# Performance work log

Hardware: AMD Instinct MI355X
Metric: run time of the kernel (lower is better)

Reference implementation:

```python
import jax, jax.numpy as jnp
import numpy as np

N_V = 100000   # vertices
N_E = 20000    # hyperedges
N_PAIRS = 1600000  # incidence pairs
F = 128
H = 128
EPS = 1e-5


def setup_inputs() -> dict:
    key = jax.random.key(0)
    k1, k2, k3, k4 = jax.random.split(key, 4)
    X = jax.random.normal(k1, (N_V, F), dtype=jnp.float32)
    vertex_ids = jax.random.randint(k2, (N_PAIRS,), 0, N_V, dtype=jnp.int32)
    edge_ids = jax.random.randint(k3, (N_PAIRS,), 0, N_E, dtype=jnp.int32)
    W = jax.random.normal(k4, (F, H), dtype=jnp.float32) * (1.0 / np.sqrt(F))
    b = jnp.zeros((H,), dtype=jnp.float32)
    gamma = jnp.ones((H,), dtype=jnp.float32)
    beta = jnp.zeros((H,), dtype=jnp.float32)
    return {"X": X, "vertex_ids": vertex_ids, "edge_ids": edge_ids,
            "W": W, "b": b, "gamma": gamma, "beta": beta}


def _segment_mean(vals, ids, num_segments):
    s = jax.ops.segment_sum(vals, ids, num_segments=num_segments)
    cnt = jax.ops.segment_sum(jnp.ones((ids.shape[0], 1), vals.dtype), ids,
                              num_segments=num_segments)
    return s / jnp.maximum(cnt, 1.0)


def reference(X, vertex_ids, edge_ids, W, b, gamma, beta):
    # linear: theta
    h = X @ W + b                                    # [N_V, H]
    # batchnorm (batch statistics, as in training mode)
    mu = jnp.mean(h, axis=0)
    var = jnp.var(h, axis=0)
    h = (h - mu) * jax.lax.rsqrt(var + EPS) * gamma + beta
    # hypergraph v2v mean: vertex -> hyperedge mean, then hyperedge -> vertex mean
    Xe = _segment_mean(h[vertex_ids], edge_ids, N_E)   # [N_E, H]
    Xv = _segment_mean(Xe[edge_ids], vertex_ids, N_V)  # [N_V, H]
    # activation (ReLU); dropout is identity in eval
    return jax.nn.relu(Xv)
```

## Files before the change

### kernel.cpp

```cpp
#include <hip/hip_runtime.h>
#include <hip/hip_bf16.h>

#define N_V 100000
#define N_E 20000
#define N_P 1600000
#define FDIM 128
#define HDIM 128
#define BN_EPS 1e-5f

#define SORT_C 4096
#define SORT_BLOCKS ((N_P + SORT_C - 1) / SORT_C)
#define NB_E 313
#define EB_SHIFT 6
#define EB_REGION 9216
#define EB_SORT 5888
#define NB_V 391
#define VB_SHIFT 8
#define VB_REGION 8192
#define VB_SORT 4608
#define SENTINEL 0xFFFFFFFFu

#define EIDX_CAP 192
#define VIDX_CAP 64

typedef __attribute__((ext_vector_type(8))) short short8;
typedef __attribute__((ext_vector_type(4))) float floatx4;

__device__ __forceinline__ float bf_lo(unsigned u) {
    return __uint_as_float(u << 16);
}
__device__ __forceinline__ float bf_hi(unsigned u) {
    return __uint_as_float(u & 0xffff0000u);
}
__device__ __forceinline__ unsigned short f2bf(float f) {
    unsigned u = __float_as_uint(f);
    return (unsigned short)((u + 0x7fffu + ((u >> 16) & 1u)) >> 16);
}

__device__ __forceinline__ void acc4(float* s, const uint2& u) {
    s[0] += bf_lo(u.x); s[1] += bf_hi(u.x);
    s[2] += bf_lo(u.y); s[3] += bf_hi(u.y);
}

__device__ __forceinline__ void acc8(float* s, const uint4& u) {
    s[0] += bf_lo(u.x); s[1] += bf_hi(u.x);
    s[2] += bf_lo(u.y); s[3] += bf_hi(u.y);
    s[4] += bf_lo(u.z); s[5] += bf_hi(u.z);
    s[6] += bf_lo(u.w); s[7] += bf_hi(u.w);
}

#define GEMM_BLOCKS 625
#define WT_STRIDE 136
__global__ __launch_bounds__(256) void k_gemm_mfma(
    const float* __restrict__ X, const float* __restrict__ W,
    const float* __restrict__ bias, unsigned* __restrict__ h_u) {
    __shared__ unsigned short WTs[FDIM * WT_STRIDE];
    const int t = threadIdx.x;
    for (int idx = t; idx < FDIM * HDIM; idx += 256) {
        const int k = idx >> 7, m = idx & 127;
        WTs[m * WT_STRIDE + k] = f2bf(W[idx]);
    }
    __syncthreads();

    const int wave = t >> 6, lane = t & 63;
    const int quad = lane >> 4, sub = lane & 15;
    const int nstrips = N_V / 16;

    for (int s = blockIdx.x * 4 + wave; s < nstrips; s += GEMM_BLOCKS * 4) {
        const int row0 = s * 16;
        short8 xf[4];
        const float* xp = X + (size_t)(row0 + sub) * FDIM + quad * 8;
        #pragma unroll
        for (int kt = 0; kt < 4; ++kt) {
            const float4 a = *(const float4*)(xp + kt * 32);
            const float4 b2 = *(const float4*)(xp + kt * 32 + 4);
            short8 f;
            f[0] = (short)f2bf(a.x);  f[1] = (short)f2bf(a.y);
            f[2] = (short)f2bf(a.z);  f[3] = (short)f2bf(a.w);
            f[4] = (short)f2bf(b2.x); f[5] = (short)f2bf(b2.y);
            f[6] = (short)f2bf(b2.z); f[7] = (short)f2bf(b2.w);
            xf[kt] = f;
        }
        #pragma unroll
        for (int tile = 0; tile < 8; ++tile) {
            floatx4 acc = {0.f, 0.f, 0.f, 0.f};
            const unsigned short* wp =
                WTs + (tile * 16 + sub) * WT_STRIDE + quad * 8;
            #pragma unroll
            for (int kt = 0; kt < 4; ++kt) {
                const short8 af = *(const short8*)(wp + kt * 32);
                acc = __builtin_amdgcn_mfma_f32_16x16x32_bf16(af, xf[kt], acc,
                                                              0, 0, 0);
            }
            const int ch = tile * 16 + quad * 4;
            const float4 bb = *(const float4*)(bias + ch);
            const float c0 = acc[0] + bb.x, c1 = acc[1] + bb.y;
            const float c2 = acc[2] + bb.z, c3 = acc[3] + bb.w;
            const unsigned lo = (unsigned)f2bf(c0) | ((unsigned)f2bf(c1) << 16);
            const unsigned hi = (unsigned)f2bf(c2) | ((unsigned)f2bf(c3) << 16);
            uint2* dst = (uint2*)(h_u + (size_t)(row0 + sub) * 64 + (ch >> 1));
            *dst = make_uint2(lo, hi);
        }
    }
}

#define BN_BLOCKS 400
#define BN_RPB 250
__global__ __launch_bounds__(256) void k_bn_stats(
    const unsigned* __restrict__ h_u, float* __restrict__ sums ) {
    const int t = threadIdx.x;
    const int c8 = t & 15;
    const int rw = t >> 4;
    const int r0 = blockIdx.x * BN_RPB;
    const int r1 = min(r0 + BN_RPB, N_V);
    float s[8] = {0.f,0.f,0.f,0.f,0.f,0.f,0.f,0.f};
    float ss[8] = {0.f,0.f,0.f,0.f,0.f,0.f,0.f,0.f};
    for (int r = r0 + rw; r < r1; r += 16) {
        const uint4 u = *(const uint4*)(h_u + (size_t)r * 64 + c8 * 4);
        const float x0 = bf_lo(u.x), x1 = bf_hi(u.x);
        const float x2 = bf_lo(u.y), x3 = bf_hi(u.y);
        const float x4 = bf_lo(u.z), x5 = bf_hi(u.z);
        const float x6 = bf_lo(u.w), x7 = bf_hi(u.w);
        s[0]+=x0; ss[0]+=x0*x0;  s[1]+=x1; ss[1]+=x1*x1;
        s[2]+=x2; ss[2]+=x2*x2;  s[3]+=x3; ss[3]+=x3*x3;
        s[4]+=x4; ss[4]+=x4*x4;  s[5]+=x5; ss[5]+=x5*x5;
        s[6]+=x6; ss[6]+=x6*x6;  s[7]+=x7; ss[7]+=x7*x7;
    }
    #pragma unroll
    for (int k = 0; k < 8; ++k) {
        s[k]  += __shfl_xor(s[k], 16);  s[k]  += __shfl_xor(s[k], 32);
        ss[k] += __shfl_xor(ss[k], 16); ss[k] += __shfl_xor(ss[k], 32);
    }
    __shared__ float ls[128], lss[128];
    for (int k = t; k < 128; k += 256) { ls[k] = 0.f; lss[k] = 0.f; }
    __syncthreads();
    if ((t & 63) < 16) {
        #pragma unroll
        for (int k = 0; k < 8; ++k) {
            atomicAdd(&ls[c8 * 8 + k], s[k]);
            atomicAdd(&lss[c8 * 8 + k], ss[k]);
        }
    }
    __syncthreads();
    if (t < 128) {
        atomicAdd(&sums[t],       ls[t]);
        atomicAdd(&sums[128 + t], lss[t]);
    }
}

__global__ void k_bn_final(const float* __restrict__ sums,
                           const float* __restrict__ gamma,
                           const float* __restrict__ beta,
                           float* __restrict__ scale, float* __restrict__ shift) {
    const int c = threadIdx.x;
    const float inv_n = 1.0f / (float)N_V;
    const float mu  = sums[c] * inv_n;
    const float var = sums[128 + c] * inv_n - mu * mu;
    const float inv = rsqrtf(var + BN_EPS);
    const float sc  = gamma[c] * inv;
    scale[c] = sc;
    shift[c] = beta[c] - mu * sc;
}

__global__ __launch_bounds__(256) void k_sort_dual(
    const int* __restrict__ vid, const int* __restrict__ eid,
    int* __restrict__ gcntE, int* __restrict__ gcntV,
    unsigned* __restrict__ partE, unsigned* __restrict__ partV) {
    __shared__ unsigned stageE[SORT_C];
    __shared__ unsigned stageV[SORT_C];
    __shared__ int histE[NB_E], curE[NB_E], offsE[NB_E], gbaseE[NB_E];
    __shared__ int histV[NB_V], curV[NB_V], offsV[NB_V], gbaseV[NB_V];
    __shared__ int partial[256];
    const int t = threadIdx.x;
    const int p0 = blockIdx.x * SORT_C;
    const int n = min(SORT_C, N_P - p0);
    const int n4 = n >> 2;
    const int4* e4p = (const int4*)(eid + p0);
    const int4* v4p = (const int4*)(vid + p0);

    for (int k = t; k < NB_E; k += 256) histE[k] = 0;
    for (int k = t; k < NB_V; k += 256) histV[k] = 0;
    __syncthreads();
    for (int i = t; i < n4; i += 256) {
        const int4 e4 = e4p[i];
        const int4 v4 = v4p[i];
        atomicAdd(&histE[((unsigned)e4.x) >> EB_SHIFT], 1);
        atomicAdd(&histE[((unsigned)e4.y) >> EB_SHIFT], 1);
        atomicAdd(&histE[((unsigned)e4.z) >> EB_SHIFT], 1);
        atomicAdd(&histE[((unsigned)e4.w) >> EB_SHIFT], 1);
        atomicAdd(&histV[((unsigned)v4.x) >> VB_SHIFT], 1);
        atomicAdd(&histV[((unsigned)v4.y) >> VB_SHIFT], 1);
        atomicAdd(&histV[((unsigned)v4.z) >> VB_SHIFT], 1);
        atomicAdd(&histV[((unsigned)v4.w) >> VB_SHIFT], 1);
    }
    __syncthreads();
    {
        constexpr int G = (NB_E + 255) / 256;
        int loc[G]; int s = 0;
        #pragma unroll
        for (int g = 0; g < G; ++g) {
            int idx = t * G + g; loc[g] = s;
            if (idx < NB_E) s += histE[idx];
        }
        partial[t] = s;
        __syncthreads();
        for (int d = 1; d < 256; d <<= 1) {
            int x = (t >= d) ? partial[t - d] : 0;
            __syncthreads(); partial[t] += x; __syncthreads();
        }
        const int base = t ? partial[t - 1] : 0;
        #pragma unroll
        for (int g = 0; g < G; ++g) {
            int idx = t * G + g;
            if (idx < NB_E) { offsE[idx] = base + loc[g]; curE[idx] = base + loc[g]; }
        }
        __syncthreads();
    }
    {
        constexpr int G = (NB_V + 255) / 256;
        int loc[G]; int s = 0;
        #pragma unroll
        for (int g = 0; g < G; ++g) {
            int idx = t * G + g; loc[g] = s;
            if (idx < NB_V) s += histV[idx];
        }
        partial[t] = s;
        __syncthreads();
        for (int d = 1; d < 256; d <<= 1) {
            int x = (t >= d) ? partial[t - d] : 0;
            __syncthreads(); partial[t] += x; __syncthreads();
        }
        const int base = t ? partial[t - 1] : 0;
        #pragma unroll
        for (int g = 0; g < G; ++g) {
            int idx = t * G + g;
            if (idx < NB_V) { offsV[idx] = base + loc[g]; curV[idx] = base + loc[g]; }
        }
        __syncthreads();
    }
    for (int i = t; i < n4; i += 256) {
        const int4 e4 = e4p[i];
        const int4 v4 = v4p[i];
        #pragma unroll
        for (int q = 0; q < 4; ++q) {
            const int ev = (q == 0) ? e4.x : (q == 1) ? e4.y : (q == 2) ? e4.z : e4.w;
            const int vv = (q == 0) ? v4.x : (q == 1) ? v4.y : (q == 2) ? v4.z : v4.w;
            const unsigned pkE = ((unsigned)(ev & 63) << 17) | (unsigned)vv;
            stageE[atomicAdd(&curE[(unsigned)ev >> EB_SHIFT], 1)] = pkE;
            const unsigned pkV = ((unsigned)(vv & 255) << 15) | (unsigned)ev;
            stageV[atomicAdd(&curV[(unsigned)vv >> VB_SHIFT], 1)] = pkV;
        }
    }
    __syncthreads();
    for (int k = t; k < NB_E; k += 256) {
        const int c = histE[k];
        gbaseE[k] = c ? atomicAdd(&gcntE[k], (c + 15) & ~15) : 0;
    }
    for (int k = t; k < NB_V; k += 256) {
        const int c = histV[k];
        gbaseV[k] = c ? atomicAdd(&gcntV[k], (c + 15) & ~15) : 0;
    }
    __syncthreads();
    for (int k = t >> 3; k < NB_E; k += 32) {
        const int c = histE[k];
        if (c == 0) continue;
        int cpad = (c + 15) & ~15;
        const int gb = gbaseE[k];
        if (gb >= EB_REGION) continue;
        cpad = min(cpad, EB_REGION - gb);
        unsigned* dst = partE + (size_t)k * EB_REGION + gb;
        const int lo = offsE[k];
        for (int j = (t & 7) * 4; j + 3 < cpad; j += 32) {
            uint4 w;
            w.x = (j + 0 < c) ? stageE[lo + j + 0] : SENTINEL;
            w.y = (j + 1 < c) ? stageE[lo + j + 1] : SENTINEL;
            w.z = (j + 2 < c) ? stageE[lo + j + 2] : SENTINEL;
            w.w = (j + 3 < c) ? stageE[lo + j + 3] : SENTINEL;
            *(uint4*)(dst + j) = w;
        }
    }
    for (int k = t >> 3; k < NB_V; k += 32) {
        const int c = histV[k];
        if (c == 0) continue;
        int cpad = (c + 15) & ~15;
        const int gb = gbaseV[k];
        if (gb >= VB_REGION) continue;
        cpad = min(cpad, VB_REGION - gb);
        unsigned* dst = partV + (size_t)k * VB_REGION + gb;
        const int lo = offsV[k];
        for (int j = (t & 7) * 4; j + 3 < cpad; j += 32) {
            uint4 w;
            w.x = (j + 0 < c) ? stageV[lo + j + 0] : SENTINEL;
            w.y = (j + 1 < c) ? stageV[lo + j + 1] : SENTINEL;
            w.z = (j + 2 < c) ? stageV[lo + j + 2] : SENTINEL;
            w.w = (j + 3 < c) ? stageV[lo + j + 3] : SENTINEL;
            *(uint4*)(dst + j) = w;
        }
    }
}

template <int NKEY, int PACK_SHIFT, int CAP, int REGION, int STRIDE>
__global__ __launch_bounds__(256) void k_csr(
    const unsigned* __restrict__ part, const int* __restrict__ gcnt,
    int nkeys_total, int* __restrict__ segoff, int* __restrict__ segcnt,
    unsigned* __restrict__ csr) {
    __shared__ __align__(16) unsigned B[CAP];
    __shared__ int hist[NKEY], offs[NKEY + 1], cur[NKEY];
    const int bkt = blockIdx.x;
    const int t = threadIdx.x;
    const unsigned mask = (1u << PACK_SHIFT) - 1u;
    const int tot = min(gcnt[bkt], REGION);
    const int tot4 = tot >> 2;
    const unsigned* src = part + (size_t)bkt * REGION;

    for (int k = t; k < NKEY; k += 256) { hist[k] = 0; cur[k] = 0; }
    __syncthreads();
    for (int i = t; i < tot4; i += 256) {
        const uint4 a = ((const uint4*)src)[i];
        if (a.x != SENTINEL) atomicAdd(&hist[a.x >> PACK_SHIFT], 1);
        if (a.y != SENTINEL) atomicAdd(&hist[a.y >> PACK_SHIFT], 1);
        if (a.z != SENTINEL) atomicAdd(&hist[a.z >> PACK_SHIFT], 1);
        if (a.w != SENTINEL) atomicAdd(&hist[a.w >> PACK_SHIFT], 1);
    }
    for (int i = tot4 * 4 + t; i < tot; i += 256) {
        const unsigned a = src[i];
        if (a != SENTINEL) atomicAdd(&hist[a >> PACK_SHIFT], 1);
    }
    __syncthreads();
    if (t == 0) {
        int acc = 0;
        for (int k = 0; k < NKEY; ++k) { offs[k] = acc; acc += hist[k]; }
        offs[NKEY] = acc;
    }
    __syncthreads();
    for (int i = t; i < tot4; i += 256) {
        const uint4 a = ((const uint4*)src)[i];
        #pragma unroll
        for (int q = 0; q < 4; ++q) {
            const unsigned av = (q == 0) ? a.x : (q == 1) ? a.y : (q == 2) ? a.z : a.w;
            if (av != SENTINEL) {
                const int k = av >> PACK_SHIFT;
                const int pos = offs[k] + atomicAdd(&cur[k], 1);
                if (pos < CAP) B[pos] = av & mask;
            }
        }
    }
    for (int i = tot4 * 4 + t; i < tot; i += 256) {
        const unsigned av = src[i];
        if (av != SENTINEL) {
            const int k = av >> PACK_SHIFT;
            const int pos = offs[k] + atomicAdd(&cur[k], 1);
            if (pos < CAP) B[pos] = av & mask;
        }
    }
    __syncthreads();
    const int total = min(offs[NKEY], CAP);
    unsigned* dst = csr + (size_t)bkt * STRIDE;
    for (int i = t * 4; i + 3 < total; i += 1024)
        *(uint4*)(dst + i) = *(const uint4*)(&B[i]);
    for (int i = (total & ~3) + t; i < total; i += 256) dst[i] = B[i];
    for (int k = t; k < NKEY; k += 256) {
        const int g = bkt * NKEY + k;
        if (g < nkeys_total) {
            const int o0 = min(offs[k], CAP);
            const int o1 = min(offs[k + 1], CAP);
            segoff[g] = bkt * STRIDE + o0;
            segcnt[g] = o1 - o0;
        }
    }
}

__global__ __launch_bounds__(256) void k_edge_gather(
    const unsigned* __restrict__ h_u, const unsigned* __restrict__ csrE,
    const int* __restrict__ eoff, const int* __restrict__ ecnt,
    const float* __restrict__ scale, const float* __restrict__ shift,
    unsigned* __restrict__ xe_u) {
    __shared__ int ib[4][EIDX_CAP];
    const int b = blockIdx.x;
    const int xcd = b & 7;
    const int half = xcd >> 2;
    const int grp = (b >> 3) * 4 + (xcd & 3);
    const int wave = threadIdx.x >> 6;
    const int e = grp * 4 + wave;
    const int l = threadIdx.x & 63;
    const int rg = l >> 4, c = l & 15;
    const int wbase = half * 32 + 2 * c;
    int o = 0, n = 0;
    if (e < N_E) { o = eoff[e]; n = ecnt[e]; }
    const int nc = min(n, EIDX_CAP);
    int* mi = ib[wave];
    for (int i = l; i < nc; i += 64) mi[i] = (int)csrE[o + i];
    __syncthreads();

    float s[4] = {0.f, 0.f, 0.f, 0.f};
    int j = 0;
    for (; j + 31 < nc; j += 32) {
        const int r0 = mi[j + rg],      r1 = mi[j + 4 + rg];
        const int r2 = mi[j + 8 + rg],  r3 = mi[j + 12 + rg];
        const int r4 = mi[j + 16 + rg], r5 = mi[j + 20 + rg];
        const int r6 = mi[j + 24 + rg], r7 = mi[j + 28 + rg];
        const uint2 u0 = *(const uint2*)(h_u + (size_t)r0 * 64 + wbase);
        const uint2 u1 = *(const uint2*)(h_u + (size_t)r1 * 64 + wbase);
        const uint2 u2 = *(const uint2*)(h_u + (size_t)r2 * 64 + wbase);
        const uint2 u3 = *(const uint2*)(h_u + (size_t)r3 * 64 + wbase);
        const uint2 u4 = *(const uint2*)(h_u + (size_t)r4 * 64 + wbase);
        const uint2 u5 = *(const uint2*)(h_u + (size_t)r5 * 64 + wbase);
        const uint2 u6 = *(const uint2*)(h_u + (size_t)r6 * 64 + wbase);
        const uint2 u7 = *(const uint2*)(h_u + (size_t)r7 * 64 + wbase);
        acc4(s, u0); acc4(s, u1); acc4(s, u2); acc4(s, u3);
        acc4(s, u4); acc4(s, u5); acc4(s, u6); acc4(s, u7);
    }
    for (; j + 15 < nc; j += 16) {
        const int r0 = mi[j + rg],     r1 = mi[j + 4 + rg];
        const int r2 = mi[j + 8 + rg], r3 = mi[j + 12 + rg];
        const uint2 u0 = *(const uint2*)(h_u + (size_t)r0 * 64 + wbase);
        const uint2 u1 = *(const uint2*)(h_u + (size_t)r1 * 64 + wbase);
        const uint2 u2 = *(const uint2*)(h_u + (size_t)r2 * 64 + wbase);
        const uint2 u3 = *(const uint2*)(h_u + (size_t)r3 * 64 + wbase);
        acc4(s, u0); acc4(s, u1); acc4(s, u2); acc4(s, u3);
    }
    for (; j < nc; j += 4) {
        if (j + rg < nc) {
            const int r = mi[j + rg];
            const uint2 u = *(const uint2*)(h_u + (size_t)r * 64 + wbase);
            acc4(s, u);
        }
    }
    for (int jj = nc; jj < n; jj += 4) {
        if (jj + rg < n) {
            const int r = (int)csrE[o + jj + rg];
            const uint2 u = *(const uint2*)(h_u + (size_t)r * 64 + wbase);
            acc4(s, u);
        }
    }
    #pragma unroll
    for (int k = 0; k < 4; ++k) {
        s[k] += __shfl_xor(s[k], 16);
        s[k] += __shfl_xor(s[k], 32);
    }
    if (e < N_E && rg == 0) {
        float m[4] = {0.f, 0.f, 0.f, 0.f};
        if (n > 0) {
            const float rc = 1.0f / (float)n;
            const float4 sc4 = ((const float4*)scale)[half * 16 + c];
            const float4 sh4 = ((const float4*)shift)[half * 16 + c];
            m[0] = sc4.x * s[0] * rc + sh4.x;
            m[1] = sc4.y * s[1] * rc + sh4.y;
            m[2] = sc4.z * s[2] * rc + sh4.z;
            m[3] = sc4.w * s[3] * rc + sh4.w;
        }
        uint2 pk;
        pk.x = (unsigned)f2bf(m[0]) | ((unsigned)f2bf(m[1]) << 16);
        pk.y = (unsigned)f2bf(m[2]) | ((unsigned)f2bf(m[3]) << 16);
        *(uint2*)(xe_u + (size_t)e * 64 + wbase) = pk;
    }
}

__global__ __launch_bounds__(256) void k_vert_gather(
    const unsigned* __restrict__ xe_u, const unsigned* __restrict__ csrV,
    const int* __restrict__ voff, const int* __restrict__ vcnt,
    float* __restrict__ out) {
    __shared__ int ib[4][VIDX_CAP];
    const int wave = threadIdx.x >> 6;
    const int v = blockIdx.x * 4 + wave;
    const int l = threadIdx.x & 63;
    const int g = l >> 4, c = l & 15;
    int o = 0, n = 0;
    if (v < N_V) { o = voff[v]; n = vcnt[v]; }
    const int nc = min(n, VIDX_CAP);
    int* mi = ib[wave];
    for (int i = l; i < nc; i += 64) mi[i] = (int)csrV[o + i];
    __syncthreads();

    float s[8] = {0.f, 0.f, 0.f, 0.f, 0.f, 0.f, 0.f, 0.f};
    int j = 0;
    for (; j + 15 < nc; j += 16) {
        const int r0 = mi[j + g],     r1 = mi[j + 4 + g];
        const int r2 = mi[j + 8 + g], r3 = mi[j + 12 + g];
        const uint4 u0 = *(const uint4*)(xe_u + (size_t)r0 * 64 + 4 * c);
        const uint4 u1 = *(const uint4*)(xe_u + (size_t)r1 * 64 + 4 * c);
        const uint4 u2 = *(const uint4*)(xe_u + (size_t)r2 * 64 + 4 * c);
        const uint4 u3 = *(const uint4*)(xe_u + (size_t)r3 * 64 + 4 * c);
        acc8(s, u0); acc8(s, u1); acc8(s, u2); acc8(s, u3);
    }
    for (; j < nc; j += 4) {
        if (j + g < nc) {
            const int r = mi[j + g];
            const uint4 u = *(const uint4*)(xe_u + (size_t)r * 64 + 4 * c);
            acc8(s, u);
        }
    }
    for (int jj = nc; jj < n; jj += 4) {
        if (jj + g < n) {
            const int r = (int)csrV[o + jj + g];
            const uint4 u = *(const uint4*)(xe_u + (size_t)r * 64 + 4 * c);
            acc8(s, u);
        }
    }
    #pragma unroll
    for (int k = 0; k < 8; ++k) {
        s[k] += __shfl_xor(s[k], 16);
        s[k] += __shfl_xor(s[k], 32);
    }
    if (v < N_V && g == 0) {
        const float rc = 1.0f / (float)max(n, 1);
        float4 r0, r1;
        r0.x = fmaxf(s[0] * rc, 0.f);
        r0.y = fmaxf(s[1] * rc, 0.f);
        r0.z = fmaxf(s[2] * rc, 0.f);
        r0.w = fmaxf(s[3] * rc, 0.f);
        r1.x = fmaxf(s[4] * rc, 0.f);
        r1.y = fmaxf(s[5] * rc, 0.f);
        r1.z = fmaxf(s[6] * rc, 0.f);
        r1.w = fmaxf(s[7] * rc, 0.f);
        ((float4*)out)[(size_t)v * 32 + 2 * c]     = r0;
        ((float4*)out)[(size_t)v * 32 + 2 * c + 1] = r1;
    }
}

extern "C" void kernel_launch(void* const* d_in, const int* in_sizes, int n_in,
                              void* d_out, int out_size, void* d_ws, size_t ws_size,
                              hipStream_t stream) {
    const float* X     = (const float*)d_in[0];
    const int*   vid   = (const int*)d_in[1];
    const int*   eid   = (const int*)d_in[2];
    const float* W     = (const float*)d_in[3];
    const float* b     = (const float*)d_in[4];
    const float* gamma = (const float*)d_in[5];
    const float* beta  = (const float*)d_in[6];
    float* out = (float*)d_out;

    char* ws = (char*)d_ws;
    unsigned* h_u   = (unsigned*)ws;  ws += (size_t)N_V * 64 * 4;
    unsigned* xe_u  = (unsigned*)ws;  ws += (size_t)N_E * 64 * 4;
    unsigned* partE = (unsigned*)ws;  ws += (size_t)NB_E * EB_REGION * 4;
    unsigned* partV = (unsigned*)ws;  ws += (size_t)NB_V * VB_REGION * 4;
    unsigned* csrE  = (unsigned*)ws;  ws += (size_t)NB_E * EB_SORT * 4;
    unsigned* csrV  = (unsigned*)ws;  ws += (size_t)NB_V * VB_SORT * 4;
    int* eoff = (int*)ws;             ws += (size_t)N_E * 4;
    int* ecnt = (int*)ws;             ws += (size_t)N_E * 4;
    int* voff = (int*)ws;             ws += (size_t)N_V * 4;
    int* vcnt = (int*)ws;             ws += (size_t)N_V * 4;
    char* zbase = ws;
    int*   gcntE = (int*)ws;          ws += (size_t)NB_E * 4;
    int*   gcntV = (int*)ws;          ws += (size_t)NB_V * 4;
    float* sums  = (float*)ws;        ws += 256 * 4;
    float* scale = (float*)ws;        ws += 128 * 4;
    float* shift = (float*)ws;        ws += 128 * 4;

    hipMemsetAsync(zbase, 0, (size_t)((char*)scale - zbase), stream);

    k_gemm_mfma<<<GEMM_BLOCKS, 256, 0, stream>>>(X, W, b, h_u);
    k_bn_stats<<<BN_BLOCKS, 256, 0, stream>>>(h_u, sums);
    k_bn_final<<<1, 128, 0, stream>>>(sums, gamma, beta, scale, shift);

    k_sort_dual<<<SORT_BLOCKS, 256, 0, stream>>>(vid, eid, gcntE, gcntV,
                                                 partE, partV);

    k_csr<64, 17, EB_SORT, EB_REGION, EB_SORT>
        <<<NB_E, 256, 0, stream>>>(partE, gcntE, N_E, eoff, ecnt, csrE);
    k_csr<256, 15, VB_SORT, VB_REGION, VB_SORT>
        <<<NB_V, 256, 0, stream>>>(partV, gcntV, N_V, voff, vcnt, csrV);

    k_edge_gather<<<(N_E / 4) * 2, 256, 0, stream>>>(h_u, csrE, eoff, ecnt,
                                                     scale, shift, xe_u);
    k_vert_gather<<<(N_V + 3) / 4, 256, 0, stream>>>(xe_u, csrV, voff, vcnt,
                                                     out);
}
```

Baseline: 285.3 us.

## Merge independent GEMM/sort and BN-stats/CSR stages into shared launches

Combines the GEMM kernel with the dual bucket-sort kernel into one launch whose blocks take one role or the other by block index, and likewise merges BN statistics with both CSR builds. Shared memory is overlaid with unions sized to the larger role. The aim is to cut launch count and let independent work fill the GPU at the same time rather than serialising small grids. The trade-off is that every block reserves the larger shared-memory footprint, which may reduce occupancy for the lighter role, and the mixed workloads may contend for memory bandwidth.

Result: faster. 259.2 us (-9.2%).

```diff
diff --git a/kernel.cpp b/kernel.cpp
--- a/kernel.cpp
+++ b/kernel.cpp
@@ -23,6 +23,11 @@
 #define EIDX_CAP 192
 #define VIDX_CAP 64
 
+#define GEMM_BLOCKS 625
+#define WT_STRIDE 136
+#define BN_BLOCKS 400
+#define BN_RPB 250
+
 typedef __attribute__((ext_vector_type(8))) short short8;
 typedef __attribute__((ext_vector_type(4))) float floatx4;
 
@@ -49,12 +54,36 @@
     s[6] += bf_lo(u.w); s[7] += bf_hi(u.w);
 }
 
-#define GEMM_BLOCKS 625
-#define WT_STRIDE 136
-__global__ __launch_bounds__(256) void k_gemm_mfma(
-    const float* __restrict__ X, const float* __restrict__ W,
-    const float* __restrict__ bias, unsigned* __restrict__ h_u) {
-    __shared__ unsigned short WTs[FDIM * WT_STRIDE];
+union SmemGemmSort {
+    struct {
+        unsigned short WTs[FDIM * WT_STRIDE];
+    } g;
+    struct {
+        unsigned stageE[SORT_C];
+        unsigned stageV[SORT_C];
+        int histE[NB_E], curE[NB_E], offsE[NB_E], gbaseE[NB_E];
+        int histV[NB_V], curV[NB_V], offsV[NB_V], gbaseV[NB_V];
+        int partial[256];
+    } s;
+};
+
+union SmemBnCsr {
+    struct {
+        unsigned B[EB_SORT];
+        int hist[256];
+        int offs[257];
+        int cur[256];
+    } c;
+    struct {
+        float ls[128], lss[128];
+    } b;
+};
+
+__device__ void gemm_body(int bid, unsigned short* WTs,
+                          const float* __restrict__ X,
+                          const float* __restrict__ W,
+                          const float* __restrict__ bias,
+                          unsigned* __restrict__ h_u) {
     const int t = threadIdx.x;
     for (int idx = t; idx < FDIM * HDIM; idx += 256) {
         const int k = idx >> 7, m = idx & 127;
@@ -66,7 +95,7 @@
     const int quad = lane >> 4, sub = lane & 15;
     const int nstrips = N_V / 16;
 
-    for (int s = blockIdx.x * 4 + wave; s < nstrips; s += GEMM_BLOCKS * 4) {
+    for (int s = bid * 4 + wave; s < nstrips; s += GEMM_BLOCKS * 4) {
         const int row0 = s * 16;
         short8 xf[4];
         const float* xp = X + (size_t)(row0 + sub) * FDIM + quad * 8;
@@ -104,75 +133,21 @@
     }
 }
 
-#define BN_BLOCKS 400
-#define BN_RPB 250
-__global__ __launch_bounds__(256) void k_bn_stats(
-    const unsigned* __restrict__ h_u, float* __restrict__ sums ) {
+__device__ void sort_body(int bid, SmemGemmSort* sm,
+                          const int* __restrict__ vid,
+                          const int* __restrict__ eid,
+                          int* __restrict__ gcntE, int* __restrict__ gcntV,
+                          unsigned* __restrict__ partE,
+                          unsigned* __restrict__ partV) {
+    unsigned* stageE = sm->s.stageE;
+    unsigned* stageV = sm->s.stageV;
+    int* histE = sm->s.histE; int* curE = sm->s.curE;
+    int* offsE = sm->s.offsE; int* gbaseE = sm->s.gbaseE;
+    int* histV = sm->s.histV; int* curV = sm->s.curV;
+    int* offsV = sm->s.offsV; int* gbaseV = sm->s.gbaseV;
+    int* partial = sm->s.partial;
     const int t = threadIdx.x;
-    const int c8 = t & 15;
-    const int rw = t >> 4;
-    const int r0 = blockIdx.x * BN_RPB;
-    const int r1 = min(r0 + BN_RPB, N_V);
-    float s[8] = {0.f,0.f,0.f,0.f,0.f,0.f,0.f,0.f};
-    float ss[8] = {0.f,0.f,0.f,0.f,0.f,0.f,0.f,0.f};
-    for (int r = r0 + rw; r < r1; r += 16) {
-        const uint4 u = *(const uint4*)(h_u + (size_t)r * 64 + c8 * 4);
-        const float x0 = bf_lo(u.x), x1 = bf_hi(u.x);
-        const float x2 = bf_lo(u.y), x3 = bf_hi(u.y);
-        const float x4 = bf_lo(u.z), x5 = bf_hi(u.z);
-        const float x6 = bf_lo(u.w), x7 = bf_hi(u.w);
-        s[0]+=x0; ss[0]+=x0*x0;  s[1]+=x1; ss[1]+=x1*x1;
-        s[2]+=x2; ss[2]+=x2*x2;  s[3]+=x3; ss[3]+=x3*x3;
-        s[4]+=x4; ss[4]+=x4*x4;  s[5]+=x5; ss[5]+=x5*x5;
-        s[6]+=x6; ss[6]+=x6*x6;  s[7]+=x7; ss[7]+=x7*x7;
-    }
-    #pragma unroll
-    for (int k = 0; k < 8; ++k) {
-        s[k]  += __shfl_xor(s[k], 16);  s[k]  += __shfl_xor(s[k], 32);
-        ss[k] += __shfl_xor(ss[k], 16); ss[k] += __shfl_xor(ss[k], 32);
-    }
-    __shared__ float ls[128], lss[128];
-    for (int k = t; k < 128; k += 256) { ls[k] = 0.f; lss[k] = 0.f; }
-    __syncthreads();
-    if ((t & 63) < 16) {
-        #pragma unroll
-        for (int k = 0; k < 8; ++k) {
-            atomicAdd(&ls[c8 * 8 + k], s[k]);
-            atomicAdd(&lss[c8 * 8 + k], ss[k]);
-        }
-    }
-    __syncthreads();
-    if (t < 128) {
-        atomicAdd(&sums[t],       ls[t]);
-        atomicAdd(&sums[128 + t], lss[t]);
-    }
-}
-
-__global__ void k_bn_final(const float* __restrict__ sums,
-                           const float* __restrict__ gamma,
-                           const float* __restrict__ beta,
-                           float* __restrict__ scale, float* __restrict__ shift) {
-    const int c = threadIdx.x;
-    const float inv_n = 1.0f / (float)N_V;
-    const float mu  = sums[c] * inv_n;
-    const float var = sums[128 + c] * inv_n - mu * mu;
-    const float inv = rsqrtf(var + BN_EPS);
-    const float sc  = gamma[c] * inv;
-    scale[c] = sc;
-    shift[c] = beta[c] - mu * sc;
-}
-
-__global__ __launch_bounds__(256) void k_sort_dual(
-    const int* __restrict__ vid, const int* __restrict__ eid,
-    int* __restrict__ gcntE, int* __restrict__ gcntV,
-    unsigned* __restrict__ partE, unsigned* __restrict__ partV) {
-    __shared__ unsigned stageE[SORT_C];
-    __shared__ unsigned stageV[SORT_C];
-    __shared__ int histE[NB_E], curE[NB_E], offsE[NB_E], gbaseE[NB_E];
-    __shared__ int histV[NB_V], curV[NB_V], offsV[NB_V], gbaseV[NB_V];
-    __shared__ int partial[256];
-    const int t = threadIdx.x;
-    const int p0 = blockIdx.x * SORT_C;
+    const int p0 = bid * SORT_C;
     const int n = min(SORT_C, N_P - p0);
     const int n4 = n >> 2;
     const int4* e4p = (const int4*)(eid + p0);
@@ -299,14 +274,68 @@
     }
 }
 
+__global__ __launch_bounds__(256) void k_gemm_sort(
+    const float* __restrict__ X, const float* __restrict__ W,
+    const float* __restrict__ bias, unsigned* __restrict__ h_u,
+    const int* __restrict__ vid, const int* __restrict__ eid,
+    int* __restrict__ gcntE, int* __restrict__ gcntV,
+    unsigned* __restrict__ partE, unsigned* __restrict__ partV) {
+    __shared__ __align__(16) SmemGemmSort sm;
+    const int b = blockIdx.x;
+    if (b < GEMM_BLOCKS)
+        gemm_body(b, sm.g.WTs, X, W, bias, h_u);
+    else
+        sort_body(b - GEMM_BLOCKS, &sm, vid, eid, gcntE, gcntV, partE, partV);
+}
+
+__device__ void bn_body(int bid, float* ls, float* lss,
+                        const unsigned* __restrict__ h_u,
+                        float* __restrict__ sums) {
+    const int t = threadIdx.x;
+    const int c8 = t & 15;
+    const int rw = t >> 4;
+    const int r0 = bid * BN_RPB;
+    const int r1 = min(r0 + BN_RPB, N_V);
+    float s[8] = {0.f,0.f,0.f,0.f,0.f,0.f,0.f,0.f};
+    float ss[8] = {0.f,0.f,0.f,0.f,0.f,0.f,0.f,0.f};
+    for (int r = r0 + rw; r < r1; r += 16) {
+        const uint4 u = *(const uint4*)(h_u + (size_t)r * 64 + c8 * 4);
+        const float x0 = bf_lo(u.x), x1 = bf_hi(u.x);
+        const float x2 = bf_lo(u.y), x3 = bf_hi(u.y);
+        const float x4 = bf_lo(u.z), x5 = bf_hi(u.z);
+        const float x6 = bf_lo(u.w), x7 = bf_hi(u.w);
+        s[0]+=x0; ss[0]+=x0*x0;  s[1]+=x1; ss[1]+=x1*x1;
+        s[2]+=x2; ss[2]+=x2*x2;  s[3]+=x3; ss[3]+=x3*x3;
+        s[4]+=x4; ss[4]+=x4*x4;  s[5]+=x5; ss[5]+=x5*x5;
+        s[6]+=x6; ss[6]+=x6*x6;  s[7]+=x7; ss[7]+=x7*x7;
+    }
+    #pragma unroll
+    for (int k = 0; k < 8; ++k) {
+        s[k]  += __shfl_xor(s[k], 16);  s[k]  += __shfl_xor(s[k], 32);
+        ss[k] += __shfl_xor(ss[k], 16); ss[k] += __shfl_xor(ss[k], 32);
+    }
+    for (int k = t; k < 128; k += 256) { ls[k] = 0.f; lss[k] = 0.f; }
+    __syncthreads();
+    if ((t & 63) < 16) {
+        #pragma unroll
+        for (int k = 0; k < 8; ++k) {
+            atomicAdd(&ls[c8 * 8 + k], s[k]);
+            atomicAdd(&lss[c8 * 8 + k], ss[k]);
+        }
+    }
+    __syncthreads();
+    if (t < 128) {
+        atomicAdd(&sums[t],       ls[t]);
+        atomicAdd(&sums[128 + t], lss[t]);
+    }
+}
+
 template <int NKEY, int PACK_SHIFT, int CAP, int REGION, int STRIDE>
-__global__ __launch_bounds__(256) void k_csr(
-    const unsigned* __restrict__ part, const int* __restrict__ gcnt,
-    int nkeys_total, int* __restrict__ segoff, int* __restrict__ segcnt,
-    unsigned* __restrict__ csr) {
-    __shared__ __align__(16) unsigned B[CAP];
-    __shared__ int hist[NKEY], offs[NKEY + 1], cur[NKEY];
-    const int bkt = blockIdx.x;
+__device__ void csr_body(int bkt, const unsigned* __restrict__ part,
+                         const int* __restrict__ gcnt, int nkeys_total,
+                         int* __restrict__ segoff, int* __restrict__ segcnt,
+                         unsigned* __restrict__ csr,
+                         unsigned* B, int* hist, int* offs, int* cur) {
     const int t = threadIdx.x;
     const unsigned mask = (1u << PACK_SHIFT) - 1u;
     const int tot = min(gcnt[bkt], REGION);
@@ -368,6 +397,41 @@
             segcnt[g] = o1 - o0;
         }
     }
+}
+
+__global__ __launch_bounds__(256) void k_bn_csr(
+    const unsigned* __restrict__ h_u, float* __restrict__ sums,
+    const unsigned* __restrict__ partE, const int* __restrict__ gcntE,
+    int* __restrict__ eoff, int* __restrict__ ecnt, unsigned* __restrict__ csrE,
+    const unsigned* __restrict__ partV, const int* __restrict__ gcntV,
+    int* __restrict__ voff, int* __restrict__ vcnt, unsigned* __restrict__ csrV) {
+    __shared__ __align__(16) SmemBnCsr sm;
+    const int b = blockIdx.x;
+    if (b < BN_BLOCKS) {
+        bn_body(b, sm.b.ls, sm.b.lss, h_u, sums);
+    } else if (b < BN_BLOCKS + NB_E) {
+        csr_body<64, 17, EB_SORT, EB_REGION, EB_SORT>(
+            b - BN_BLOCKS, partE, gcntE, N_E, eoff, ecnt, csrE,
+            sm.c.B, sm.c.hist, sm.c.offs, sm.c.cur);
+    } else {
+        csr_body<256, 15, VB_SORT, VB_REGION, VB_SORT>(
+            b - BN_BLOCKS - NB_E, partV, gcntV, N_V, voff, vcnt, csrV,
+            sm.c.B, sm.c.hist, sm.c.offs, sm.c.cur);
+    }
+}
+
+__global__ void k_bn_final(const float* __restrict__ sums,
+                           const float* __restrict__ gamma,
+                           const float* __restrict__ beta,
+                           float* __restrict__ scale, float* __restrict__ shift) {
+    const int c = threadIdx.x;
+    const float inv_n = 1.0f / (float)N_V;
+    const float mu  = sums[c] * inv_n;
+    const float var = sums[128 + c] * inv_n - mu * mu;
+    const float inv = rsqrtf(var + BN_EPS);
+    const float sc  = gamma[c] * inv;
+    scale[c] = sc;
+    shift[c] = beta[c] - mu * sc;
 }
 
 __global__ __launch_bounds__(256) void k_edge_gather(
@@ -550,17 +614,14 @@
 
     hipMemsetAsync(zbase, 0, (size_t)((char*)scale - zbase), stream);
 
-    k_gemm_mfma<<<GEMM_BLOCKS, 256, 0, stream>>>(X, W, b, h_u);
-    k_bn_stats<<<BN_BLOCKS, 256, 0, stream>>>(h_u, sums);
+    k_gemm_sort<<<GEMM_BLOCKS + SORT_BLOCKS, 256, 0, stream>>>(
+        X, W, b, h_u, vid, eid, gcntE, gcntV, partE, partV);
+
+    k_bn_csr<<<BN_BLOCKS + NB_E + NB_V, 256, 0, stream>>>(
+        h_u, sums, partE, gcntE, eoff, ecnt, csrE,
+        partV, gcntV, voff, vcnt, csrV);
+
     k_bn_final<<<1, 128, 0, stream>>>(sums, gamma, beta, scale, shift);
-
-    k_sort_dual<<<SORT_BLOCKS, 256, 0, stream>>>(vid, eid, gcntE, gcntV,
-                                                 partE, partV);
-
-    k_csr<64, 17, EB_SORT, EB_REGION, EB_SORT>
-        <<<NB_E, 256, 0, stream>>>(partE, gcntE, N_E, eoff, ecnt, csrE);
-    k_csr<256, 15, VB_SORT, VB_REGION, VB_SORT>
-        <<<NB_V, 256, 0, stream>>>(partV, gcntV, N_V, voff, vcnt, csrV);
 
     k_edge_gather<<<(N_E / 4) * 2, 256, 0, stream>>>(h_u, csrE, eoff, ecnt,
                                                      scale, shift, xe_u);
```
